# Performance work log

Hardware: AMD Instinct MI355X
Metric: run time of the kernel (lower is better)

The kernel has to match this reference:

```python
import jax, jax.numpy as jnp
import numpy as np

CH = 128
KSIZE = 7
BS, H, W = 8, 56, 56


def nbhd_extract(x, k):
    """Faithful replication of square_nbhd_extractor(k)(x) from the torch code,
    including its permute(0,2,1).reshape(bs,h,w,d) layout reinterpretation and
    the unfold over the last two dims of that layout. x: (bs, n, d) -> (bs, n, k*k, d)."""
    bs, n, d = x.shape
    h = w = int(np.sqrt(n))
    # torch: x.permute(0,2,1).reshape(bs,h,w,d)
    y = jnp.transpose(x, (0, 2, 1)).reshape(bs, h, w, d)
    # extract_image_patches treats y as (b, c=h, H=w, W=d); stride=1, dilation=1
    # pad both sliding dims by k-1 total ((k-1)//2 low, rest high)
    p_lo = (k - 1) // 2
    p_hi = (k - 1) - p_lo
    yp = jnp.pad(y, ((0, 0), (0, 0), (p_lo, p_hi), (p_lo, p_hi)))
    Hs, Ws = w, d  # output sliding sizes equal original dims (stride 1)
    # double unfold: window over dim2 at axis -2, window over dim3 at axis -1
    wins = jnp.stack([
        jnp.stack([yp[:, :, i:i + Hs, j:j + Ws] for j in range(k)], axis=-1)
        for i in range(k)], axis=-2)  # (bs, h, w, d, k, k)
    patches = jnp.transpose(wins, (0, 4, 5, 1, 2, 3))  # (bs, k, k, h, w, d)
    # torch: patches.view(bs, n, d, r).permute(0,1,3,2)
    return patches.reshape(bs, n, d, k * k).transpose(0, 1, 3, 2)  # (bs, n, r, d)


def setup_inputs() -> dict:
    key = jax.random.key(0)
    ks = jax.random.split(key, 3)
    x = jax.random.normal(ks[0], (BS, CH, H, W), dtype=jnp.float32)
    W1 = jax.random.normal(ks[1], (2, CH), dtype=jnp.float32) * np.float32(1.0 / np.sqrt(2.0))
    b1 = jnp.zeros((CH,), dtype=jnp.float32)
    W2 = jax.random.normal(ks[2], (CH, CH), dtype=jnp.float32) * np.float32(1.0 / np.sqrt(CH))
    b2 = jnp.zeros((CH,), dtype=jnp.float32)
    return {"x": x, "W1": W1, "b1": b1, "W2": W2, "b2": b2, "ksize": KSIZE}


def reference(x, W1, b1, W2, b2, ksize):
    bs, c, h, w = x.shape
    n = h * w
    # coords: meshgrid('ij') of linspace(-3,3), shape (1, n, 2)
    gi = jnp.linspace(-3.0, 3.0, h)
    gj = jnp.linspace(-3.0, 3.0, w)
    coords = jnp.stack(jnp.meshgrid(gi, gj, indexing='ij'), axis=-1).reshape(1, n, 2)
    rel = nbhd_extract(coords, ksize) - coords[:, :, None, :]  # (1, n, r, 2)
    # position MLP: Linear(2,ch) -> ReLU -> Linear(ch,ch)
    P = jax.nn.relu(rel @ W1 + b1) @ W2 + b2                   # (1, n, r, ch)
    Wsm = jax.nn.softmax(P, axis=2)[0]                          # (n, r, c) ; ch == c
    # values: gather neighborhood patches of channels-last points
    xp = jnp.transpose(x, (0, 2, 3, 1)).reshape(bs, n, c)
    V = nbhd_extract(xp, ksize)                                 # (bs, n, r, c)
    # head-folded weighting * value reduce over neighborhood == per-channel weighted sum
    out = jnp.einsum('nrc,bnrc->bnc', Wsm, V)                   # (bs, n, c)
    return jnp.transpose(out, (0, 2, 1)).reshape(bs, c, h, w)
```

## Files before the change

kernel.cpp:

```cpp
#include <hip/hip_runtime.h>

#define CH   128
#define KS   7
#define R    49
#define HH   56
#define NPOS 3136
#define BS   8
#define XSTR 401408
#define XTOT (BS*XSTR)

typedef short short8 __attribute__((ext_vector_type(8)));
typedef float f32x4  __attribute__((ext_vector_type(4)));
typedef unsigned int u32;
typedef u32 u32x4 __attribute__((ext_vector_type(4)));

__device__ __forceinline__ short f2bf(float f) {
    unsigned u = __float_as_uint(f);
    u += 0x7fffu + ((u >> 16) & 1u);
    return (short)(u >> 16);
}
__device__ __forceinline__ float bf2f(short s) {
    return __uint_as_float(((unsigned)(unsigned short)s) << 16);
}
__device__ __forceinline__ float bf2f_u(u32 lo16) {
    return __uint_as_float(lo16 << 16);
}

#define HSTR 136
#define PSTR 132
#define WGT_PP 3200
#define WPL  789
#define NCHK 785

__global__ __launch_bounds__(256) void poatt_prep(
    const float* __restrict__ W2, short* __restrict__ wsH, short* __restrict__ wsL)
{
    int t = blockIdx.x * 256 + threadIdx.x;
    int k = t >> 7, ch = t & 127;
    float w = W2[k * CH + ch];
    short hi = f2bf(w);
    wsH[ch * CH + k] = hi;
    wsL[ch * CH + k] = f2bf(w - bf2f(hi));
}

__global__ __launch_bounds__(256) void poatt_cvt(
    const float* __restrict__ x, u32* __restrict__ x2)
{
    int t = blockIdx.x * 256 + threadIdx.x;
    const float4* xv = reinterpret_cast<const float4*>(x);
    float4 a = xv[2 * t], b = xv[2 * t + 1];
    u32x4 o;
    o[0] = (u32)(unsigned short)f2bf(a.x) | ((u32)(unsigned short)f2bf(a.y) << 16);
    o[1] = (u32)(unsigned short)f2bf(a.z) | ((u32)(unsigned short)f2bf(a.w) << 16);
    o[2] = (u32)(unsigned short)f2bf(b.x) | ((u32)(unsigned short)f2bf(b.y) << 16);
    o[3] = (u32)(unsigned short)f2bf(b.z) | ((u32)(unsigned short)f2bf(b.w) << 16);
    reinterpret_cast<u32x4*>(x2)[t] = o;
}

__global__ __launch_bounds__(256, 4) void poatt_fused(
    const u32* __restrict__ x2,
    const float* __restrict__ W1, const float* __restrict__ b1,
    const short* __restrict__ wsH, const short* __restrict__ wsL,
    float* __restrict__ trb)
{
    __shared__ float rel_s[R][2];
    __shared__ float part_s[CH];
    __shared__ u32 wpack[25 * CH];
    __shared__ __align__(16) char smem[64 * HSTR * 2];
    short* hid_s = (short*)smem;
    u32*   win   = (u32*)smem;

    const int pos = blockIdx.x;
    const int tid = threadIdx.x;
    const int ch  = tid & (CH - 1);
    const int g   = tid >> 7;

    const int q  = pos >> 6;
    const int s  = pos & 63;
    const int ii = q / KS;
    const int jj = q % KS;

    if (tid < 2 * R) {
        const int e  = (tid >= R) ? 1 : 0;
        const int rr = tid - e * R;
        int F  = (pos * 2 + e) * R + rr;
        int ep = F & 1;
        int t  = F >> 1;
        int jp = t % HH; t /= HH;
        int a  = t % HH; t /= HH;
        int jc = t % KS;
        int ic = t / KS;
        int row = jp + ic - 3;
        int col = ep + jc - 3;
        float v = 0.0f;
        if (row >= 0 && row < HH && (col == 0 || col == 1)) {
            int f    = a * (HH * 2) + row * 2 + col;
            int cidx = f / NPOS;
            int p    = f - cidx * NPOS;
            int u    = (cidx == 0) ? (p / HH) : (p % HH);
            v = -3.0f + 6.0f * (float)u * (1.0f / 55.0f);
        }
        const float c0 = -3.0f + 6.0f * (float)(pos / HH) * (1.0f / 55.0f);
        const float c1 = -3.0f + 6.0f * (float)(pos % HH) * (1.0f / 55.0f);
        rel_s[rr][e] = v - ((e == 0) ? c0 : c1);
    }
    __syncthreads();

    {
        const float w10 = W1[ch];
        const float w11 = W1[CH + ch];
        const float bb  = b1[ch];
        for (int rr = g; rr < R; rr += 2) {
            float h = fmaf(rel_s[rr][0], w10, fmaf(rel_s[rr][1], w11, bb));
            hid_s[rr * HSTR + ch] = f2bf(fmaxf(h, 0.0f));
        }
        for (int t = tid; t < 15 * HSTR; t += 256) hid_s[R * HSTR + t] = 0;
    }
    __syncthreads();

    const int winbase = s * (R * CH) + (ii - 3) * CH + (jj - 3);
    const int m2v = winbase & 1;
    const int hw  = winbase >> 1;
    const int m3  = hw & 3;
    const int cw0 = (hw - m3) >> 2;
    const u32x4* x2v = reinterpret_cast<const u32x4*>(x2);
    const unsigned short* x2s = reinterpret_cast<const unsigned short*>(x2);

    u32x4 v[4];
    auto ld = [&](int b) {
        const int cb = cw0 + b * (XSTR >> 3);
        const bool safe = (b > 0 || winbase >= 8) && (b < BS - 1 || winbase + 6280 <= XSTR);
        if (safe) {
            v[0] = x2v[cb + tid];
            v[1] = x2v[cb + tid + 256];
            v[2] = x2v[cb + tid + 512];
            if (tid < NCHK - 768) v[3] = x2v[cb + tid + 768];
        } else {
            #pragma unroll
            for (int j = 0; j < 4; ++j) {
                if (j < 3 || tid < NCHK - 768) {
                    int dwx = 4 * (cb + tid + 256 * j);
                    u32x4 o;
                    #pragma unroll
                    for (int k = 0; k < 4; ++k) {
                        int g0 = 2 * (dwx + k);
                        int g1 = g0 + 1;
                        g0 = g0 < 0 ? 0 : (g0 >= XTOT ? XTOT - 1 : g0);
                        g1 = g1 < 0 ? 0 : (g1 >= XTOT ? XTOT - 1 : g1);
                        o[k] = (u32)x2s[g0] | ((u32)x2s[g1] << 16);
                    }
                    v[j] = o;
                }
            }
        }
    };
    auto st = [&]() {
        #pragma unroll
        for (int j = 0; j < 4; ++j) {
            if (j < 3 || tid < NCHK - 768) {
                int u = tid + 256 * j;
                win[0 * WPL + u] = v[j][0];
                win[1 * WPL + u] = v[j][1];
                win[2 * WPL + u] = v[j][2];
                win[3 * WPL + u] = v[j][3];
            }
        }
    };

    ld(0);

    const int w  = tid >> 6;
    const int l  = tid & 63;
    const int lr = l & 15;
    const int kg = l >> 4;

    f32x4 acc[4][2];
    #pragma unroll
    for (int mt = 0; mt < 4; ++mt) { acc[mt][0] = (f32x4)0.0f; acc[mt][1] = (f32x4)0.0f; }

    #pragma unroll
    for (int np = 0; np < 2; ++np) {
        const int bcol = 32 * w + 16 * np + lr;
        short8 bH[4], bL[4];
        #pragma unroll
        for (int kk = 0; kk < 4; ++kk) {
            bH[kk] = *reinterpret_cast<const short8*>(wsH + bcol * CH + kk * 32 + kg * 8);
            bL[kk] = *reinterpret_cast<const short8*>(wsL + bcol * CH + kk * 32 + kg * 8);
        }
        #pragma unroll
        for (int mt = 0; mt < 4; ++mt) {
            #pragma unroll
            for (int kk = 0; kk < 4; ++kk) {
                short8 a = *reinterpret_cast<const short8*>(
                    &hid_s[(16 * mt + lr) * HSTR + kk * 32 + kg * 8]);
                acc[mt][np] = __builtin_amdgcn_mfma_f32_16x16x32_bf16(a, bH[kk], acc[mt][np], 0, 0, 0);
                acc[mt][np] = __builtin_amdgcn_mfma_f32_16x16x32_bf16(a, bL[kk], acc[mt][np], 0, 0, 0);
            }
        }
    }

    {
        const int wb0 = s * (R * CH);
        float wv[4][4];
        #pragma unroll
        for (int np = 0; np < 2; ++np) {
            const int chh = 32 * w + 16 * np + lr;

            float mx = -1e30f;
            #pragma unroll
            for (int mt = 0; mt < 4; ++mt)
                #pragma unroll
                for (int r = 0; r < 4; ++r) {
                    int rr = 16 * mt + 4 * kg + r;
                    if (rr < R) mx = fmaxf(mx, acc[mt][np][r]);
                }
            mx = fmaxf(mx, __shfl_xor(mx, 16));
            mx = fmaxf(mx, __shfl_xor(mx, 32));

            float sm = 0.0f;
            #pragma unroll
            for (int mt = 0; mt < 4; ++mt)
                #pragma unroll
                for (int r = 0; r < 4; ++r) {
                    int rr = 16 * mt + 4 * kg + r;
                    float e = (rr < R) ? __expf(acc[mt][np][r] - mx) : 0.0f;
                    wv[mt][r] = e;
                    sm += e;
                }
            sm += __shfl_xor(sm, 16);
            sm += __shfl_xor(sm, 32);
            const float inv = 1.0f / sm;

            #pragma unroll
            for (int mt = 0; mt < 4; ++mt)
                #pragma unroll
                for (int r = 0; r < 4; ++r) {
                    int rr = 16 * mt + 4 * kg + r;
                    if (rr < R) {
                        int rem = wb0 + chh * R + rr;
                        int e2  = rem & (CH - 1);
                        int j2  = (rem >> 7) % HH;
                        int row = j2 + ii - 3;
                        int col = e2 + jj - 3;
                        bool valid = (row >= 0) && (row < HH) && (col >= 0) && (col < CH);
                        wv[mt][r] = valid ? wv[mt][r] * inv : 0.0f;
                    }
                }

            #pragma unroll
            for (int mt = 0; mt < 4; ++mt)
                #pragma unroll
                for (int jp = 0; jp < 2; ++jp) {
                    int j = 8 * mt + 2 * kg + jp;
                    if (j <= 24) {
                        u32 pk = (u32)(unsigned short)f2bf(wv[mt][2 * jp])
                               | ((u32)(unsigned short)f2bf(wv[mt][2 * jp + 1]) << 16);
                        wpack[j * CH + chh] = pk;
                    }
                }
        }
    }
    __syncthreads();

    st();

    float qw[28];
    {
        const int j0 = g ? 13 : 0;
        const int nj = g ? 12 : 13;
        u32 wr[13];
        #pragma unroll
        for (int i = 0; i < 13; ++i) wr[i] = (i < nj) ? wpack[(j0 + i) * CH + ch] : 0u;
        float pw[26];
        #pragma unroll
        for (int i = 0; i < 13; ++i) {
            pw[2 * i]     = bf2f_u(wr[i] & 0xffffu);
            pw[2 * i + 1] = bf2f_u(wr[i] >> 16);
        }
        const int kw0 = g ? 26 : 0;
        const int par = (m2v + 49 * ch + kw0) & 1;
        #pragma unroll
        for (int k2 = 0; k2 < 28; ++k2) {
            float a_ = (k2 < 26) ? pw[k2] : 0.0f;
            float b_ = (k2 >= 1 && k2 <= 26) ? pw[k2 - 1] : 0.0f;
            qw[k2] = par ? b_ : a_;
        }
    }
    const int d0 = m3 + ((m2v + 49 * ch + (g ? 26 : 0)) >> 1);
    __syncthreads();

    for (int b = 0; b < BS; ++b) {
        if (b + 1 < BS) ld(b + 1);

        float acc2 = 0.0f;
        #pragma unroll
        for (int dd = 0; dd < 14; ++dd) {
            int c = d0 + dd;
            u32 wd = win[(c & 3) * WPL + (c >> 2)];
            acc2 = fmaf(bf2f_u(wd & 0xffffu), qw[2 * dd],     acc2);
            acc2 = fmaf(bf2f_u(wd >> 16),     qw[2 * dd + 1], acc2);
        }
        if (g) part_s[ch] = acc2;
        __syncthreads();
        if (!g) trb[((size_t)b * NPOS + pos) * CH + ch] = acc2 + part_s[ch];
        if (b + 1 < BS) st();
        __syncthreads();
    }
}

__global__ __launch_bounds__(256) void poatt_tr(
    const float* __restrict__ ws, float* __restrict__ out)
{
    __shared__ float t[64 * 129];
    const int blk = blockIdx.x;
    const int b   = blk / 49;
    const int p0  = (blk % 49) * 64;
    const int tid = threadIdx.x;

    const int chR = tid & 127, pR = tid >> 7;
    #pragma unroll
    for (int r = 0; r < 32; ++r) {
        int pl = pR + 2 * r;
        t[pl * 129 + chR] = ws[((size_t)b * NPOS + p0 + pl) * CH + chR];
    }
    __syncthreads();
    const int pW = tid & 63, chW0 = tid >> 6;
    #pragma unroll
    for (int c = 0; c < 32; ++c) {
        int chl = chW0 + 4 * c;
        out[((size_t)b * CH + chl) * NPOS + p0 + pW] = t[pW * 129 + chl];
    }
}

template<bool WS_W2, bool USE_WS>
__global__ __launch_bounds__(256, 4) void poatt_mono(
    const float* __restrict__ x,
    const float* __restrict__ W1, const float* __restrict__ b1,
    const float* __restrict__ W2,
    const short* __restrict__ wsH, const short* __restrict__ wsL,
    float* __restrict__ dst)
{
    __shared__ float rel_s[R][2];
    __shared__ __align__(16) char smem[2 * 64 * HSTR * 2];
    short* hidH = (short*)smem;
    short* hidL = hidH + 64 * HSTR;
    float* Pbuf = (float*)smem;

    const int pos = blockIdx.x;
    const int tid = threadIdx.x;
    const int ch  = tid & (CH - 1);
    const int g   = tid >> 7;

    const int q  = pos >> 6;
    const int ii = q / KS;
    const int jj = q % KS;

    if (tid < 2 * R) {
        const int e  = (tid >= R) ? 1 : 0;
        const int rr = tid - e * R;
        int F  = (pos * 2 + e) * R + rr;
        int ep = F & 1;
        int t  = F >> 1;
        int jp = t % HH; t /= HH;
        int a  = t % HH; t /= HH;
        int jc = t % KS;
        int ic = t / KS;
        int row = jp + ic - 3;
        int col = ep + jc - 3;
        float v = 0.0f;
        if (row >= 0 && row < HH && (col == 0 || col == 1)) {
            int f    = a * (HH * 2) + row * 2 + col;
            int cidx = f / NPOS;
            int p    = f - cidx * NPOS;
            int u    = (cidx == 0) ? (p / HH) : (p % HH);
            v = -3.0f + 6.0f * (float)u * (1.0f / 55.0f);
        }
        const float c0 = -3.0f + 6.0f * (float)(pos / HH) * (1.0f / 55.0f);
        const float c1 = -3.0f + 6.0f * (float)(pos % HH) * (1.0f / 55.0f);
        rel_s[rr][e] = v - ((e == 0) ? c0 : c1);
    }
    __syncthreads();

    {
        const float w10 = W1[ch];
        const float w11 = W1[CH + ch];
        const float bb  = b1[ch];
        for (int rr = g; rr < R; rr += 2) {
            float h = fmaf(rel_s[rr][0], w10, fmaf(rel_s[rr][1], w11, bb));
            h = fmaxf(h, 0.0f);
            short hi = f2bf(h);
            hidH[rr * HSTR + ch] = hi;
            hidL[rr * HSTR + ch] = f2bf(h - bf2f(hi));
        }
        for (int t = tid; t < 15 * HSTR; t += 256) {
            hidH[R * HSTR + t] = 0;
            hidL[R * HSTR + t] = 0;
        }
    }
    __syncthreads();

    {
        const int w  = tid >> 6;
        const int l  = tid & 63;
        const int lr = l & 15;
        const int kg = l >> 4;

        short8 aH[4], aL[4];
        const int abase = (16 * w + lr) * HSTR + kg * 8;
        #pragma unroll
        for (int kk = 0; kk < 4; ++kk) {
            aH[kk] = *reinterpret_cast<const short8*>(&hidH[abase + kk * 32]);
            aL[kk] = *reinterpret_cast<const short8*>(&hidL[abase + kk * 32]);
        }

        f32x4 acc[8];
        #pragma unroll
        for (int n = 0; n < 8; ++n) acc[n] = (f32x4)0.0f;

        #pragma unroll
        for (int n = 0; n < 8; ++n) {
            const int bcol = 16 * n + lr;
            #pragma unroll
            for (int kk = 0; kk < 4; ++kk) {
                short8 bH, bL;
                if (WS_W2) {
                    bH = *reinterpret_cast<const short8*>(wsH + bcol * CH + kk * 32 + kg * 8);
                    bL = *reinterpret_cast<const short8*>(wsL + bcol * CH + kk * 32 + kg * 8);
                } else {
                    #pragma unroll
                    for (int j = 0; j < 8; ++j) {
                        float ww = ((const float*)W2)[(kk * 32 + kg * 8 + j) * CH + bcol];
                        short hi = f2bf(ww);
                        bH[j] = hi;
                        bL[j] = f2bf(ww - bf2f(hi));
                    }
                }
                acc[n] = __builtin_amdgcn_mfma_f32_16x16x32_bf16(aL[kk], bH, acc[n], 0, 0, 0);
                acc[n] = __builtin_amdgcn_mfma_f32_16x16x32_bf16(aH[kk], bL, acc[n], 0, 0, 0);
                acc[n] = __builtin_amdgcn_mfma_f32_16x16x32_bf16(aH[kk], bH, acc[n], 0, 0, 0);
            }
        }
        __syncthreads();

        #pragma unroll
        for (int n = 0; n < 8; ++n) {
            #pragma unroll
            for (int r = 0; r < 4; ++r) {
                int rr = 16 * w + kg * 4 + r;
                if (rr < R) Pbuf[rr * PSTR + 16 * n + lr] = acc[n][r];
            }
        }
    }
    __syncthreads();

    if (tid < CH) {
        float p[R];
        #pragma unroll
        for (int rr = 0; rr < R; ++rr) p[rr] = Pbuf[rr * PSTR + tid];
        float mx = p[0];
        #pragma unroll
        for (int rr = 1; rr < R; ++rr) mx = fmaxf(mx, p[rr]);
        float s = 0.0f;
        #pragma unroll
        for (int rr = 0; rr < R; ++rr) { p[rr] = __expf(p[rr] - mx); s += p[rr]; }
        const float inv = 1.0f / s;
        const int wb0 = (pos & 63) * (R * CH);
        #pragma unroll
        for (int rr = 0; rr < R; ++rr) {
            int rem = wb0 + tid * R + rr;
            int e2  = rem & (CH - 1);
            int j2  = (rem >> 7) % HH;
            int row = j2 + ii - 3;
            int col = e2 + jj - 3;
            bool valid = (row >= 0) && (row < HH) && (col >= 0) && (col < CH);
            Pbuf[rr * PSTR + tid] = valid ? p[rr] * inv : 0.0f;
        }
    }
    __syncthreads();

    float p[R];
    #pragma unroll
    for (int rr = 0; rr < R; ++rr) p[rr] = Pbuf[rr * PSTR + ch];

    const int winbase = (pos & 63) * (R * CH) + (ii - 3) * CH + (jj - 3);
    const int base_t  = winbase + ch * R;

    #pragma unroll
    for (int bi = 0; bi < 4; ++bi) {
        const int b  = g * 4 + bi;
        const int ab = b * XSTR + base_t;
        const bool safe = (b > 0 || winbase >= 0) && (b < BS - 1 || winbase + R * CH <= XSTR);
        float acc = 0.0f;
        if (safe) {
            #pragma unroll
            for (int rr = 0; rr < R; ++rr) acc = fmaf(p[rr], x[ab + rr], acc);
        } else {
            #pragma unroll
            for (int rr = 0; rr < R; ++rr) {
                int a2 = ab + rr;
                a2 = a2 < 0 ? 0 : (a2 >= XTOT ? XTOT - 1 : a2);
                acc = fmaf(p[rr], x[a2], acc);
            }
        }
        if (USE_WS) dst[((size_t)b * NPOS + pos) * CH + ch] = acc;
        else        dst[((size_t)b * CH + ch) * NPOS + pos] = acc;
    }
}

extern "C" void kernel_launch(void* const* d_in, const int* in_sizes, int n_in,
                              void* d_out, int out_size, void* d_ws, size_t ws_size,
                              hipStream_t stream) {
    (void)in_sizes; (void)n_in; (void)out_size;
    const float* x  = (const float*)d_in[0];
    const float* W1 = (const float*)d_in[1];
    const float* b1 = (const float*)d_in[2];
    const float* W2 = (const float*)d_in[3];
    float* out = (float*)d_out;

    const size_t W2T_BYTES = 2u * CH * CH * sizeof(short);
    const size_t X2_BYTES  = (size_t)XTOT * 2;
    const size_t TRB_BYTES = (size_t)BS * NPOS * CH * sizeof(float);
    const size_t FULL = W2T_BYTES + X2_BYTES + TRB_BYTES;

    short* wsH = (short*)d_ws;
    short* wsL = wsH + CH * CH;

    if (ws_size >= FULL) {
        u32*   x2  = (u32*)((char*)d_ws + W2T_BYTES);
        float* trb = (float*)((char*)d_ws + W2T_BYTES + X2_BYTES);

        poatt_prep<<<dim3(64), dim3(256), 0, stream>>>(W2, wsH, wsL);
        poatt_cvt<<<dim3(XTOT / (256 * 8)), dim3(256), 0, stream>>>(x, x2);
        poatt_fused<<<dim3(NPOS), dim3(256), 0, stream>>>(x2, W1, b1, wsH, wsL, trb);
        poatt_tr<<<dim3(BS * 49), dim3(256), 0, stream>>>(trb, out);
    } else if (ws_size >= W2T_BYTES + TRB_BYTES) {
        float* trb = (float*)((char*)d_ws + W2T_BYTES);
        poatt_prep<<<dim3(64), dim3(256), 0, stream>>>(W2, wsH, wsL);
        poatt_mono<true, true><<<dim3(NPOS), dim3(256), 0, stream>>>(
            x, W1, b1, W2, wsH, wsL, trb);
        poatt_tr<<<dim3(BS * 49), dim3(256), 0, stream>>>(trb, out);
    } else if (ws_size >= W2T_BYTES) {
        poatt_prep<<<dim3(64), dim3(256), 0, stream>>>(W2, wsH, wsL);
        poatt_mono<true, false><<<dim3(NPOS), dim3(256), 0, stream>>>(
            x, W1, b1, W2, wsH, wsL, out);
    } else {
        poatt_mono<false, false><<<dim3(NPOS), dim3(256), 0, stream>>>(
            x, W1, b1, W2, nullptr, nullptr, out);
    }
}
```

Baseline: 78.29 us.

## Process two batches per iteration with double window buffers and full-row dots

The per-batch window loop now stages two batches at once into separate shared buffers: the hidden/MLP buffer is reused for one and the packed-weight buffer for the other. Each thread group handles one batch and computes the full 49-tap dot product itself, rather than splitting the taps across the two 128-thread halves and merging partials through shared memory. This halves the number of barriers and removes the partial-sum exchange. Window stores become contiguous 16-byte writes in place of strided 4-byte scatters. In exchange, register use rises (two prefetch buffers plus 50 weight floats) and the shared reads per thread become unaligned scalar loads over 25 words.

After: 87.12 us. +11.3%, slower.

```diff
diff --git a/kernel.cpp b/kernel.cpp
--- a/kernel.cpp
+++ b/kernel.cpp
@@ -22,15 +22,10 @@
 __device__ __forceinline__ float bf2f(short s) {
     return __uint_as_float(((unsigned)(unsigned short)s) << 16);
 }
-__device__ __forceinline__ float bf2f_u(u32 lo16) {
-    return __uint_as_float(lo16 << 16);
-}
 
 #define HSTR 136
 #define PSTR 132
-#define WGT_PP 3200
-#define WPL  789
-#define NCHK 785
+#define NWIN 3140
 
 __global__ __launch_bounds__(256) void poatt_prep(
     const float* __restrict__ W2, short* __restrict__ wsH, short* __restrict__ wsL)
@@ -64,11 +59,12 @@
     float* __restrict__ trb)
 {
     __shared__ float rel_s[R][2];
-    __shared__ float part_s[CH];
-    __shared__ u32 wpack[25 * CH];
-    __shared__ __align__(16) char smem[64 * HSTR * 2];
-    short* hid_s = (short*)smem;
-    u32*   win   = (u32*)smem;
+    __shared__ __align__(16) char smemA[64 * HSTR * 2];
+    __shared__ __align__(16) char smemB[25 * CH * 4];
+    short* hid_s = (short*)smemA;
+    u32*   wpack = (u32*)smemB;
+    u32*   win0  = (u32*)smemA;
+    u32*   win1  = (u32*)smemB;
 
     const int pos = blockIdx.x;
     const int tid = threadIdx.x;
@@ -119,60 +115,53 @@
     __syncthreads();
 
     const int winbase = s * (R * CH) + (ii - 3) * CH + (jj - 3);
-    const int m2v = winbase & 1;
     const int hw  = winbase >> 1;
     const int m3  = hw & 3;
     const int cw0 = (hw - m3) >> 2;
     const u32x4* x2v = reinterpret_cast<const u32x4*>(x2);
     const unsigned short* x2s = reinterpret_cast<const unsigned short*>(x2);
 
-    u32x4 v[4];
-    auto ld = [&](int b) {
-        const int cb = cw0 + b * (XSTR >> 3);
+    u32x4 vA[4], vB[4];
+    auto ldbuf = [&](int b, u32x4* v) {
         const bool safe = (b > 0 || winbase >= 8) && (b < BS - 1 || winbase + 6280 <= XSTR);
+        const int cb = b * (XSTR >> 3) + cw0;
         if (safe) {
             v[0] = x2v[cb + tid];
             v[1] = x2v[cb + tid + 256];
             v[2] = x2v[cb + tid + 512];
-            if (tid < NCHK - 768) v[3] = x2v[cb + tid + 768];
+            if (tid < 17) v[3] = x2v[cb + tid + 768];
         } else {
             #pragma unroll
             for (int j = 0; j < 4; ++j) {
-                if (j < 3 || tid < NCHK - 768) {
-                    int dwx = 4 * (cb + tid + 256 * j);
+                if (j < 3 || tid < 17) {
+                    int gc = cb + tid + 256 * j;
                     u32x4 o;
                     #pragma unroll
-                    for (int k = 0; k < 4; ++k) {
-                        int g0 = 2 * (dwx + k);
-                        int g1 = g0 + 1;
-                        g0 = g0 < 0 ? 0 : (g0 >= XTOT ? XTOT - 1 : g0);
-                        g1 = g1 < 0 ? 0 : (g1 >= XTOT ? XTOT - 1 : g1);
-                        o[k] = (u32)x2s[g0] | ((u32)x2s[g1] << 16);
+                    for (int kk = 0; kk < 4; ++kk) {
+                        int e0 = 8 * gc + 2 * kk;
+                        int a0 = e0;     a0 = a0 < 0 ? 0 : (a0 >= XTOT ? XTOT - 1 : a0);
+                        int a1 = e0 + 1; a1 = a1 < 0 ? 0 : (a1 >= XTOT ? XTOT - 1 : a1);
+                        o[kk] = (u32)x2s[a0] | ((u32)x2s[a1] << 16);
                     }
                     v[j] = o;
                 }
             }
         }
     };
-    auto st = [&]() {
-        #pragma unroll
-        for (int j = 0; j < 4; ++j) {
-            if (j < 3 || tid < NCHK - 768) {
-                int u = tid + 256 * j;
-                win[0 * WPL + u] = v[j][0];
-                win[1 * WPL + u] = v[j][1];
-                win[2 * WPL + u] = v[j][2];
-                win[3 * WPL + u] = v[j][3];
-            }
-        }
+    auto stbuf = [&](const u32x4* v, u32* wb) {
+        *reinterpret_cast<u32x4*>(&wb[4 * tid])         = v[0];
+        *reinterpret_cast<u32x4*>(&wb[4 * (tid + 256)]) = v[1];
+        *reinterpret_cast<u32x4*>(&wb[4 * (tid + 512)]) = v[2];
+        if (tid < 17)
+            *reinterpret_cast<u32x4*>(&wb[4 * (tid + 768)]) = v[3];
     };
 
-    ld(0);
-
-    const int w  = tid >> 6;
-    const int l  = tid & 63;
-    const int lr = l & 15;
-    const int kg = l >> 4;
+    ldbuf(0, vA);
+
+    const int wv_ = tid >> 6;
+    const int l   = tid & 63;
+    const int lr  = l & 15;
+    const int kg  = l >> 4;
 
     f32x4 acc[4][2];
     #pragma unroll
@@ -180,7 +169,7 @@
 
     #pragma unroll
     for (int np = 0; np < 2; ++np) {
-        const int bcol = 32 * w + 16 * np + lr;
+        const int bcol = 32 * wv_ + 16 * np + lr;
         short8 bH[4], bL[4];
         #pragma unroll
         for (int kk = 0; kk < 4; ++kk) {
@@ -204,7 +193,7 @@
         float wv[4][4];
         #pragma unroll
         for (int np = 0; np < 2; ++np) {
-            const int chh = 32 * w + 16 * np + lr;
+            const int chh = 32 * wv_ + 16 * np + lr;
 
             float mx = -1e30f;
             #pragma unroll
@@ -262,49 +251,49 @@
     }
     __syncthreads();
 
-    st();
-
-    float qw[28];
+    ldbuf(1, vB);
+
+    const int p_ = (winbase + 49 * ch) & 1;
+    float qlo[25], qhi[25];
     {
-        const int j0 = g ? 13 : 0;
-        const int nj = g ? 12 : 13;
-        u32 wr[13];
-        #pragma unroll
-        for (int i = 0; i < 13; ++i) wr[i] = (i < nj) ? wpack[(j0 + i) * CH + ch] : 0u;
-        float pw[26];
-        #pragma unroll
-        for (int i = 0; i < 13; ++i) {
-            pw[2 * i]     = bf2f_u(wr[i] & 0xffffu);
-            pw[2 * i + 1] = bf2f_u(wr[i] >> 16);
-        }
-        const int kw0 = g ? 26 : 0;
-        const int par = (m2v + 49 * ch + kw0) & 1;
-        #pragma unroll
-        for (int k2 = 0; k2 < 28; ++k2) {
-            float a_ = (k2 < 26) ? pw[k2] : 0.0f;
-            float b_ = (k2 >= 1 && k2 <= 26) ? pw[k2 - 1] : 0.0f;
-            qw[k2] = par ? b_ : a_;
-        }
-    }
-    const int d0 = m3 + ((m2v + 49 * ch + (g ? 26 : 0)) >> 1);
-    __syncthreads();
-
-    for (int b = 0; b < BS; ++b) {
-        if (b + 1 < BS) ld(b + 1);
-
+        u32 wr2[25];
+        #pragma unroll
+        for (int i = 0; i < 25; ++i) wr2[i] = wpack[i * CH + ch];
+        #pragma unroll
+        for (int i = 0; i < 25; ++i) {
+            u32 qp = p_ ? ((wr2[i] << 16) | (i ? (wr2[i - 1] >> 16) : 0u)) : wr2[i];
+            qlo[i] = __uint_as_float(qp << 16);
+            qhi[i] = __uint_as_float(qp & 0xffff0000u);
+        }
+    }
+
+    stbuf(vA, win0);
+    __syncthreads();
+    stbuf(vB, win1);
+    ldbuf(2, vA);
+    ldbuf(3, vB);
+    __syncthreads();
+
+    const int base_l = ((winbase + 49 * ch) >> 1) - (hw - m3);
+    const u32* wb = g ? win1 : win0;
+
+    for (int k = 0; k < 4; ++k) {
         float acc2 = 0.0f;
         #pragma unroll
-        for (int dd = 0; dd < 14; ++dd) {
-            int c = d0 + dd;
-            u32 wd = win[(c & 3) * WPL + (c >> 2)];
-            acc2 = fmaf(bf2f_u(wd & 0xffffu), qw[2 * dd],     acc2);
-            acc2 = fmaf(bf2f_u(wd >> 16),     qw[2 * dd + 1], acc2);
-        }
-        if (g) part_s[ch] = acc2;
-        __syncthreads();
-        if (!g) trb[((size_t)b * NPOS + pos) * CH + ch] = acc2 + part_s[ch];
-        if (b + 1 < BS) st();
-        __syncthreads();
+        for (int d = 0; d < 25; ++d) {
+            u32 wd = wb[base_l + d];
+            acc2 = fmaf(__uint_as_float(wd << 16),          qlo[d], acc2);
+            acc2 = fmaf(__uint_as_float(wd & 0xffff0000u),  qhi[d], acc2);
+        }
+        trb[((size_t)(2 * k + g) * NPOS + pos) * CH + ch] = acc2;
+
+        if (k < 3) {
+            __syncthreads();
+            stbuf(vA, win0);
+            stbuf(vB, win1);
+            if (k < 2) { ldbuf(2 * k + 4, vA); ldbuf(2 * k + 5, vB); }
+            __syncthreads();
+        }
     }
 }
 
```
